# Kernel optimization log

Hardware: AMD Instinct MI355X
Metric: run time of the kernel (lower is better)

Reference implementation:

```python
import jax, jax.numpy as jnp
import numpy as np

CHUNK = 256
ROPE_BASE = 10000.0
EPS = 1e-6


def setup_inputs() -> dict:
    key = jax.random.key(0)
    ks = jax.random.split(key, 8)
    B, N, D, H, K = 4, 8192, 1024, 16, 4
    x = jax.random.normal(ks[0], (B, N, D), dtype=jnp.float32)
    norm_scale = jnp.ones((D,), dtype=jnp.float32)
    conv_w = jax.random.normal(ks[1], (D, 1, K), dtype=jnp.float32) * 0.2
    conv_b = jax.random.normal(ks[2], (D,), dtype=jnp.float32) * 0.02
    in_proj_w = jax.random.normal(ks[3], (D, 3 * D), dtype=jnp.float32) * 0.02
    dt_bias = jax.random.normal(ks[4], (D,), dtype=jnp.float32) * 0.5
    head_mix = jnp.eye(H, dtype=jnp.float32) + 0.02 * jax.random.normal(ks[5], (H, H), dtype=jnp.float32)
    out_proj_w = jax.random.normal(ks[6], (D, D), dtype=jnp.float32) * 0.02
    return {"x": x, "norm_scale": norm_scale, "conv_w": conv_w, "conv_b": conv_b,
            "in_proj_w": in_proj_w, "dt_bias": dt_bias, "head_mix": head_mix,
            "out_proj_w": out_proj_w}


def _rmsnorm(x, scale):
    xf = x.astype(jnp.float32)
    rms = jax.lax.rsqrt(jnp.mean(xf * xf, axis=-1, keepdims=True) + EPS)
    out = scale.astype(jnp.float32) * (xf * rms)
    return jnp.clip(out, -60000.0, 60000.0).astype(x.dtype)


def _rope(v, N, d_head, dtype):
    # v: (B, N, H, d_head); cos/sin: (N, d_head//2)
    half = d_head // 2
    inv_freq = 1.0 / (ROPE_BASE ** (jnp.arange(0, d_head, 2, dtype=jnp.float32) / d_head))
    freqs = jnp.arange(N, dtype=jnp.float32)[:, None] * inv_freq[None, :]
    cos = jnp.cos(freqs).astype(dtype)[None, :, None, :]
    sin = jnp.sin(freqs).astype(dtype)[None, :, None, :]
    v1, v2 = v[..., :half], v[..., half:]
    return jnp.concatenate([v1 * cos - v2 * sin, v1 * sin + v2 * cos], axis=-1)


def reference(x, norm_scale, conv_w, conv_b, in_proj_w, dt_bias, head_mix, out_proj_w):
    residual = x
    B, N, D = x.shape
    H = head_mix.shape[0]
    d_head = D // H
    xn = _rmsnorm(x, norm_scale)

    # depthwise causal conv: torch pads K-1 both sides then truncates to N -> left-pad only
    K = conv_w.shape[-1]
    xc = jax.lax.conv_general_dilated(
        xn.transpose(0, 2, 1), conv_w, window_strides=(1,), padding=[(K - 1, 0)],
        feature_group_count=D, dimension_numbers=("NCH", "OIH", "NCH"))
    xc = (xc + conv_b[None, :, None]).transpose(0, 2, 1)  # (B, N, D)
    xc = xc * jax.nn.sigmoid(xc)  # SiLU

    fused = xc @ in_proj_w  # (B, N, 3D)
    dt_raw, v, gate_raw = jnp.split(fused, 3, axis=-1)
    dt = jnp.clip(jax.nn.softplus(dt_raw.astype(jnp.float32) + dt_bias.astype(jnp.float32)),
                  0.001, 2.0).astype(dt_raw.dtype)
    gate = jax.nn.sigmoid(gate_raw)
    log_alpha = -dt.astype(jnp.float32)

    v_rot = _rope(v.reshape(B, N, H, d_head), N, d_head, x.dtype).reshape(B, N, D)
    v_in = (v_rot * dt).astype(jnp.float32)

    # pad to multiple of CHUNK (static)
    pad = (-N) % CHUNK
    if pad:
        v_in = jnp.pad(v_in, ((0, 0), (0, pad), (0, 0)))
        log_alpha = jnp.pad(log_alpha, ((0, 0), (0, pad), (0, 0)))
    Np = N + pad
    nc = Np // CHUNK
    v_ch = v_in.reshape(B, nc, CHUNK, D)
    la_ch = log_alpha.reshape(B, nc, CHUNK, D)

    # intra-chunk stabilized cumulative scan
    L = jnp.clip(jnp.cumsum(la_ch, axis=2), -20.0, 0.0)
    L_max = jnp.max(L, axis=2, keepdims=True)
    L_st = L - L_max
    cum_scaled = jnp.cumsum(jnp.exp(-L_st) * v_ch, axis=2)
    chunk_out = jnp.exp(L_st) * cum_scaled  # (B, nc, CHUNK, D)

    if nc > 1:
        # inter-chunk carry, fully parallel
        bdecay = L[:, :, -1, :]            # (B, nc, D)
        bout = chunk_out[:, :, -1, :]      # (B, nc, D)
        cum_decay = jnp.clip(jnp.cumsum(bdecay, axis=1), -80.0, 0.0)
        stab = jnp.max(cum_decay, axis=1, keepdims=True)
        ncd = jnp.clip(cum_decay - stab, -20.0, 0.0)
        seeds = bout * jnp.exp(-ncd)
        shifted = jnp.pad(seeds[:, :-1], ((0, 0), (1, 0), (0, 0)))
        carries = jnp.cumsum(shifted, axis=1) * jnp.exp(ncd)  # (B, nc, D)
        final = chunk_out + carries[:, :, None, :] * jnp.exp(L)
    else:
        final = chunk_out
    final = final.astype(x.dtype).reshape(B, Np, D)[:, :N, :]

    v_mix = jnp.einsum("bnhd,hm->bnmd", final.reshape(B, N, H, d_head), head_mix)
    final = v_mix.reshape(B, N, D)
    out = (final * gate) @ out_proj_w
    return residual + out
```

## Files before the change

### kernel.cpp

```cpp
#include <hip/hip_runtime.h>

#define TOK 32768
#define DMODEL 1024
#define NSEQ 8192
#define NCHK 32
#define CHUNKC 256
#define KDIM 1024
#define NKT (KDIM / 32)
#define LOG2E 1.44269504f

typedef __attribute__((ext_vector_type(8))) short bf16x8;
typedef __attribute__((ext_vector_type(4))) float f32x4;

__device__ __forceinline__ unsigned short f2bf(float f) {
  unsigned u = __float_as_uint(f);
  u += 0x7fffu + ((u >> 16) & 1u);
  return (unsigned short)(u >> 16);
}
__device__ __forceinline__ float bf2f(unsigned short h) {
  return __uint_as_float(((unsigned)h) << 16);
}
__device__ __forceinline__ float sigm(float x) {
  return __builtin_amdgcn_rcpf(1.f + exp2f(-LOG2E * x));
}

typedef __attribute__((address_space(3))) unsigned int lds_u32_t;
typedef const __attribute__((address_space(1))) unsigned int glb_u32_t;

__device__ __forceinline__ void gl_lds16(const void* g, void* l) {
  __builtin_amdgcn_global_load_lds((glb_u32_t*)g, (lds_u32_t*)l, 16, 0, 0);
}

__global__ __launch_bounds__(256) void transpose_bf16_k(const float* __restrict__ in,
                                                        unsigned short* __restrict__ out,
                                                        int R, int C) {
  __shared__ float tile[32][33];
  const int c0 = blockIdx.x * 32, r0 = blockIdx.y * 32;
  const int tx = threadIdx.x, ty = threadIdx.y;
#pragma unroll
  for (int i = 0; i < 32; i += 8)
    tile[ty + i][tx] = in[(long)(r0 + ty + i) * C + c0 + tx];
  __syncthreads();
#pragma unroll
  for (int i = 0; i < 32; i += 8)
    out[(long)(c0 + ty + i) * R + r0 + tx] = f2bf(tile[tx][ty + i]);
}

__global__ __launch_bounds__(256) void ropetab_k(float2* __restrict__ tab) {
  const int i = blockIdx.x * 256 + threadIdx.x;
  const int f = i & 31, n = i >> 5;
  const float invf = exp2f(-(float)f * (13.287712379549449f / 32.0f));
  const float ang = (float)n * invf;
  tab[i] = make_float2(cosf(ang), sinf(ang));
}

__global__ __launch_bounds__(256) void rmsconv_k(const float* __restrict__ x,
                                                 const float* __restrict__ scale,
                                                 const float* __restrict__ w,
                                                 const float* __restrict__ cb,
                                                 unsigned short* __restrict__ xc) {
  __shared__ float xs[11][1024];
  __shared__ float red[4];
  const int t = threadIdx.x;
  const long row0 = (long)blockIdx.x * 8;
  const bool seqstart = ((row0 & (NSEQ - 1)) == 0);
  const float4 sc = ((const float4*)scale)[t];
  for (int i = 0; i < 11; ++i) {
    if (i < 3 && seqstart) {
      ((float4*)xs[i])[t] = make_float4(0.f, 0.f, 0.f, 0.f);
      continue;
    }
    const long r = row0 - 3 + i;
    const float4 v = ((const float4*)(x + r * DMODEL))[t];
    float ss = v.x * v.x + v.y * v.y + v.z * v.z + v.w * v.w;
#pragma unroll
    for (int off = 32; off > 0; off >>= 1) ss += __shfl_down(ss, off);
    if ((t & 63) == 0) red[t >> 6] = ss;
    __syncthreads();
    const float tot = red[0] + red[1] + red[2] + red[3];
    const float rr = rsqrtf(tot * (1.0f / DMODEL) + 1e-6f);
    float4 o;
    o.x = fminf(fmaxf(v.x * rr * sc.x, -60000.f), 60000.f);
    o.y = fminf(fmaxf(v.y * rr * sc.y, -60000.f), 60000.f);
    o.z = fminf(fmaxf(v.z * rr * sc.z, -60000.f), 60000.f);
    o.w = fminf(fmaxf(v.w * rr * sc.w, -60000.f), 60000.f);
    ((float4*)xs[i])[t] = o;
    __syncthreads();
  }
  __syncthreads();
  const int d0 = t * 4;
  float wl[4][4];
#pragma unroll
  for (int j = 0; j < 4; ++j) {
    const float4 t4 = *(const float4*)(w + (d0 + j) * 4);
    wl[j][0] = t4.x; wl[j][1] = t4.y; wl[j][2] = t4.z; wl[j][3] = t4.w;
  }
  const float4 cb4 = ((const float4*)cb)[t];
#pragma unroll
  for (int orow = 0; orow < 8; ++orow) {
    float o[4] = {0.f, 0.f, 0.f, 0.f};
#pragma unroll
    for (int k = 0; k < 4; ++k) {
      const float4 xv = ((const float4*)xs[orow + k])[t];
      o[0] += xv.x * wl[0][k]; o[1] += xv.y * wl[1][k];
      o[2] += xv.z * wl[2][k]; o[3] += xv.w * wl[3][k];
    }
    ushort4 st;
    { const float a = o[0] + cb4.x; st.x = f2bf(a * sigm(a)); }
    { const float a = o[1] + cb4.y; st.y = f2bf(a * sigm(a)); }
    { const float a = o[2] + cb4.z; st.z = f2bf(a * sigm(a)); }
    { const float a = o[3] + cb4.w; st.w = f2bf(a * sigm(a)); }
    *(ushort4*)(xc + (row0 + orow) * DMODEL + d0) = st;
  }
}

template <int EPI, int NBN, int SBN>
__global__ __launch_bounds__(256) void gemm_bt(const unsigned short* __restrict__ A,
                                               const unsigned short* __restrict__ BT,
                                               unsigned short* __restrict__ ob,
                                               float* __restrict__ of,
                                               const float* __restrict__ resid) {
  __shared__ unsigned short As[3][128 * 32];
  __shared__ unsigned short Bs[3][256 * 32];
  const int tid = threadIdx.x;
  const int l = tid & 63;
  const int w = tid >> 6;
  constexpr int NC = (EPI == 0) ? 3072 : 1024;

  constexpr int BPS = 4 * SBN;
  constexpr int NBNS = NBN / SBN;
  const int lin = blockIdx.y * NBN + blockIdx.x;
  const int xcd = lin & 7;
  const int g = lin >> 3;
  const int s = g / BPS;
  const int r = g - s * BPS;
  const int bmo = r / SBN;
  const int bno = r - bmo * SBN;
  const int bmS = s / NBNS;
  const int bnS = s - bmS * NBNS;
  const int bm = xcd * 32 + bmS * 4 + bmo;
  const int bn = bnS * SBN + bno;

  f32x4 acc[8][4];
#pragma unroll
  for (int m = 0; m < 8; ++m)
#pragma unroll
    for (int n = 0; n < 4; ++n) acc[m][n] = {0.f, 0.f, 0.f, 0.f};

  const int srcc = (((l & 3) ^ ((l >> 3) & 3)) * 8);
  const unsigned short* aG0 = A + ((long)(bm * 128 + w * 32 + (l >> 2))) * KDIM + srcc;
  const unsigned short* bG0 = BT + ((long)(bn * 256 + w * 64 + (l >> 2))) * KDIM + srcc;
  const int aLo = (w * 32) * 32;
  const int bLo = (w * 64) * 32;

#define STAGE(buf, k0)                                           \
  {                                                              \
    gl_lds16(aG0 + (k0),             &As[buf][aLo]);             \
    gl_lds16(aG0 + (k0) + 16 * KDIM, &As[buf][aLo + 512]);       \
    gl_lds16(bG0 + (k0),             &Bs[buf][bLo]);             \
    gl_lds16(bG0 + (k0) + 16 * KDIM, &Bs[buf][bLo + 512]);       \
    gl_lds16(bG0 + (k0) + 32 * KDIM, &Bs[buf][bLo + 1024]);      \
    gl_lds16(bG0 + (k0) + 48 * KDIM, &Bs[buf][bLo + 1536]);      \
  }

  const int eoff = (((l >> 4) ^ ((l >> 1) & 3)) * 8);
  const int arow0 = (l & 15) * 32 + eoff;
  const int brow0 = (w * 64 + (l & 15)) * 32 + eoff;

  auto compute = [&](int cur) {
    const unsigned short* Ab = &As[cur][0];
    const unsigned short* Bb = &Bs[cur][0];
    bf16x8 af[8], bfr[4];
#pragma unroll
    for (int m = 0; m < 8; ++m) af[m] = *(const bf16x8*)&Ab[arow0 + m * 512];
#pragma unroll
    for (int n = 0; n < 4; ++n) bfr[n] = *(const bf16x8*)&Bb[brow0 + n * 512];
    __builtin_amdgcn_s_setprio(1);
#pragma unroll
    for (int m = 0; m < 8; ++m)
#pragma unroll
      for (int n = 0; n < 4; ++n)
        acc[m][n] = __builtin_amdgcn_mfma_f32_16x16x32_bf16(af[m], bfr[n], acc[m][n], 0, 0, 0);
    __builtin_amdgcn_s_setprio(0);
  };

  STAGE(0, 0);
  STAGE(1, 32);
  asm volatile("s_waitcnt vmcnt(6)" ::: "memory");
  int cur = 0, nxt = 2;
  for (int t = 0; t < NKT - 2; ++t) {
    __builtin_amdgcn_s_barrier();
    __builtin_amdgcn_sched_barrier(0);
    STAGE(nxt, (t + 2) * 32);
    compute(cur);
    asm volatile("s_waitcnt vmcnt(6)" ::: "memory");
    cur = (cur == 2) ? 0 : cur + 1;
    nxt = (nxt == 2) ? 0 : nxt + 1;
  }
  __builtin_amdgcn_s_barrier();
  __builtin_amdgcn_sched_barrier(0);
  compute(cur);
  asm volatile("s_waitcnt vmcnt(0)" ::: "memory");
  cur = (cur == 2) ? 0 : cur + 1;
  __builtin_amdgcn_s_barrier();
  __builtin_amdgcn_sched_barrier(0);
  compute(cur);
#undef STAGE

  const int rbase = bm * 128;
  const int cbase = bn * 256 + w * 64;
  const int lr4 = (l >> 4) * 4;
  const int lc16 = l & 15;

  if constexpr (EPI == 0) {
#pragma unroll
    for (int m = 0; m < 8; ++m)
#pragma unroll
      for (int n = 0; n < 4; ++n) {
        const int col = cbase + n * 16 + lc16;
#pragma unroll
        for (int j2 = 0; j2 < 4; ++j2) {
          const int row = rbase + m * 16 + lr4 + j2;
          ob[(long)row * NC + col] = f2bf(acc[m][n][j2]);
        }
      }
  } else {
#pragma unroll
    for (int m = 0; m < 8; ++m)
#pragma unroll
      for (int n = 0; n < 4; ++n) {
        const int col = cbase + n * 16 + lc16;
#pragma unroll
        for (int j2 = 0; j2 < 4; ++j2) {
          const int row = rbase + m * 16 + lr4 + j2;
          const long o = (long)row * NC + col;
          of[o] = resid[o] + acc[m][n][j2];
        }
      }
  }
}

__global__ __launch_bounds__(256) void scan1_k(const unsigned short* __restrict__ fu,
                                               const float* __restrict__ dt_bias,
                                               const float2* __restrict__ tab,
                                               float* __restrict__ Llast,
                                               float* __restrict__ bout) {
  const int idx = blockIdx.x * 256 + threadIdx.x;
  const int d = idx & 1023;
  const int ch = (idx >> 10) & 31;
  const int b = idx >> 15;
  const long base = ((long)b * NSEQ + ch * CHUNKC) * 3072 + d;
  const float bias = dt_bias[d];
  const int f = d & 31;
  const bool hi = (d & 32) != 0;
  const int po = hi ? -32 : 32;
  float run = 0.f, s = 0.f, L = 0.f;
#pragma unroll 4
  for (int c = 0; c < CHUNKC; ++c) {
    const long o = base + (long)c * 3072;
    const float a = bf2f(fu[o]) + bias;
    const float e2 = exp2f(-LOG2E * fabsf(a));
    const float sp = fmaxf(a, 0.f) + 0.69314718f * log2f(1.f + e2);
    const float dtv = fminf(fmaxf(sp, 0.001f), 2.0f);
    const float own = bf2f(fu[o + 1024]);
    const float oth = bf2f(fu[o + 1024 + po]);
    const float2 cs = tab[(ch * CHUNKC + c) * 32 + f];
    const float vr = own * cs.x + (hi ? oth * cs.y : -oth * cs.y);
    run -= dtv;
    L = fminf(fmaxf(run, -20.f), 0.f);
    s += exp2f(-LOG2E * L) * (vr * dtv);
  }
  Llast[idx] = L;
  bout[idx] = exp2f(LOG2E * L) * s;
}

__global__ __launch_bounds__(256) void scan2_k(const float* __restrict__ Llast,
                                               const float* __restrict__ bout,
                                               float* __restrict__ carry) {
  const int idx = blockIdx.x * 256 + threadIdx.x;
  const int d = idx & 1023;
  const int b = idx >> 10;
  const long base = (long)b * (NCHK * DMODEL) + d;
  float cd[NCHK];
  float run = 0.f, stab = -1e30f;
#pragma unroll
  for (int ch = 0; ch < NCHK; ++ch) {
    run += Llast[base + ch * DMODEL];
    cd[ch] = fminf(fmaxf(run, -80.f), 0.f);
    stab = fmaxf(stab, cd[ch]);
  }
  float acc = 0.f;
#pragma unroll
  for (int ch = 0; ch < NCHK; ++ch) {
    const float ncd = fminf(fmaxf(cd[ch] - stab, -20.f), 0.f);
    carry[base + ch * DMODEL] = acc * exp2f(LOG2E * ncd);
    acc += bout[base + ch * DMODEL] * exp2f(-LOG2E * ncd);
  }
}

__global__ __launch_bounds__(256) void scan3_k(unsigned short* fu,
                                               const float* __restrict__ dt_bias,
                                               const float2* __restrict__ tab,
                                               const float* __restrict__ carry) {
  const int idx = blockIdx.x * 256 + threadIdx.x;
  const int d = idx & 1023;
  const int ch = (idx >> 10) & 31;
  const int b = idx >> 15;
  const long base = ((long)b * NSEQ + ch * CHUNKC) * 3072 + d;
  const float bias = dt_bias[d];
  const int f = d & 31;
  const bool hi = (d & 32) != 0;
  const int po = hi ? -32 : 32;
  const float ce = carry[idx];
  float run = 0.f, s = 0.f;
#pragma unroll 4
  for (int c = 0; c < CHUNKC; ++c) {
    const long o = base + (long)c * 3072;
    const float a = bf2f(fu[o]) + bias;
    const float e2 = exp2f(-LOG2E * fabsf(a));
    const float sp = fmaxf(a, 0.f) + 0.69314718f * log2f(1.f + e2);
    const float dtv = fminf(fmaxf(sp, 0.001f), 2.0f);
    const float own = bf2f(fu[o + 1024]);
    const float oth = bf2f(fu[o + 1024 + po]);
    const float2 cs = tab[(ch * CHUNKC + c) * 32 + f];
    const float vr = own * cs.x + (hi ? oth * cs.y : -oth * cs.y);
    run -= dtv;
    const float L = fminf(fmaxf(run, -20.f), 0.f);
    s += exp2f(-LOG2E * L) * (vr * dtv);
    fu[o + 1024] = f2bf(exp2f(LOG2E * L) * (s + ce));
  }
}

__global__ __launch_bounds__(256) void headmix_k(const unsigned short* __restrict__ fu,
                                                 const float* __restrict__ hm,
                                                 unsigned short* __restrict__ A2) {
  __shared__ float mixs[256];
  const int t = threadIdx.x;
  mixs[t] = hm[t];
  __syncthreads();
  const long row = (long)blockIdx.x * 4 + (t >> 6);
  const int dd = t & 63;
  const unsigned short* fv0 = fu + row * 3072 + 1024 + dd;
  const unsigned short* gv0 = fu + row * 3072 + 2048 + dd;
  float fv[16];
#pragma unroll
  for (int h = 0; h < 16; ++h) fv[h] = bf2f(fv0[h * 64]);
#pragma unroll
  for (int m = 0; m < 16; ++m) {
    float o = 0.f;
#pragma unroll
    for (int h = 0; h < 16; ++h) o += fv[h] * mixs[h * 16 + m];
    A2[row * DMODEL + m * 64 + dd] = f2bf(o * sigm(bf2f(gv0[m * 64])));
  }
}

extern "C" void kernel_launch(void* const* d_in, const int* in_sizes, int n_in,
                              void* d_out, int out_size, void* d_ws, size_t ws_size,
                              hipStream_t stream) {
  const float* x        = (const float*)d_in[0];
  const float* nscale   = (const float*)d_in[1];
  const float* conv_w   = (const float*)d_in[2];
  const float* conv_b   = (const float*)d_in[3];
  const float* in_proj  = (const float*)d_in[4];
  const float* dt_bias  = (const float*)d_in[5];
  const float* head_mix = (const float*)d_in[6];
  const float* out_proj = (const float*)d_in[7];
  float* out = (float*)d_out;

  char* p = (char*)d_ws;
  unsigned short* W1T = (unsigned short*)p; p += (size_t)3072 * 1024 * 2;
  unsigned short* W2T = (unsigned short*)p; p += (size_t)1024 * 1024 * 2;
  float2* tab  = (float2*)p; p += (size_t)NSEQ * 32 * sizeof(float2);
  float* Llast = (float*)p;  p += (size_t)131072 * 4;
  float* bout  = (float*)p;  p += (size_t)131072 * 4;
  float* carry = (float*)p;  p += (size_t)131072 * 4;
  unsigned short* fusedb = (unsigned short*)p; p += (size_t)TOK * 3072 * 2;
  unsigned short* xc     = (unsigned short*)p; p += (size_t)TOK * DMODEL * 2;

  transpose_bf16_k<<<dim3(96, 32), dim3(32, 8), 0, stream>>>(in_proj, W1T, 1024, 3072);
  transpose_bf16_k<<<dim3(32, 32), dim3(32, 8), 0, stream>>>(out_proj, W2T, 1024, 1024);
  ropetab_k<<<1024, 256, 0, stream>>>(tab);
  rmsconv_k<<<TOK / 8, 256, 0, stream>>>(x, nscale, conv_w, conv_b, xc);

  gemm_bt<0, 12, 6><<<dim3(12, 256), 256, 0, stream>>>(xc, W1T, fusedb, nullptr, nullptr);
  scan1_k<<<512, 256, 0, stream>>>(fusedb, dt_bias, tab, Llast, bout);
  scan2_k<<<16, 256, 0, stream>>>(Llast, bout, carry);
  scan3_k<<<512, 256, 0, stream>>>(fusedb, dt_bias, tab, carry);
  headmix_k<<<TOK / 4, 256, 0, stream>>>(fusedb, head_mix, xc );
  gemm_bt<1, 4, 4><<<dim3(4, 256), 256, 0, stream>>>(xc, W2T, nullptr, out, x);
}
```

Baseline: 626.8 us.

## Enlarge GEMM tiles to 256x256 with 8 waves, fuse prep kernels, register-resident rmsconv

The GEMM moves from 128x256 tiles with 4 waves to 256x256 tiles with 8 waves arranged 2x4, with per-wave staging adjusted. This halves the grid and increases operand reuse per LDS load. The weight transposes and the rope table are merged into one prep launch. rmsconv now keeps its 11 input rows in registers and does a single barrier instead of staging through 44KB of LDS. The risks are higher register pressure and fewer blocks per CU for the GEMM.

```diff
diff --git a/kernel.cpp b/kernel.cpp
--- a/kernel.cpp
+++ b/kernel.cpp
@@ -6,7 +6,6 @@
 #define NCHK 32
 #define CHUNKC 256
 #define KDIM 1024
-#define NKT (KDIM / 32)
 #define LOG2E 1.44269504f
 
 typedef __attribute__((ext_vector_type(8))) short bf16x8;
@@ -31,27 +30,36 @@
   __builtin_amdgcn_global_load_lds((glb_u32_t*)g, (lds_u32_t*)l, 16, 0, 0);
 }
 
-__global__ __launch_bounds__(256) void transpose_bf16_k(const float* __restrict__ in,
-                                                        unsigned short* __restrict__ out,
-                                                        int R, int C) {
+__global__ __launch_bounds__(256) void prep_k(const float* __restrict__ w1,
+                                              const float* __restrict__ w2,
+                                              unsigned short* __restrict__ w1t,
+                                              unsigned short* __restrict__ w2t,
+                                              float2* __restrict__ tab) {
   __shared__ float tile[32][33];
-  const int c0 = blockIdx.x * 32, r0 = blockIdx.y * 32;
-  const int tx = threadIdx.x, ty = threadIdx.y;
-#pragma unroll
-  for (int i = 0; i < 32; i += 8)
-    tile[ty + i][tx] = in[(long)(r0 + ty + i) * C + c0 + tx];
-  __syncthreads();
-#pragma unroll
-  for (int i = 0; i < 32; i += 8)
-    out[(long)(c0 + ty + i) * R + r0 + tx] = f2bf(tile[tx][ty + i]);
-}
-
-__global__ __launch_bounds__(256) void ropetab_k(float2* __restrict__ tab) {
-  const int i = blockIdx.x * 256 + threadIdx.x;
-  const int f = i & 31, n = i >> 5;
-  const float invf = exp2f(-(float)f * (13.287712379549449f / 32.0f));
-  const float ang = (float)n * invf;
-  tab[i] = make_float2(cosf(ang), sinf(ang));
+  const int bid = blockIdx.x;
+  const int t = threadIdx.x;
+  if (bid < 4096) {
+    const float* in;
+    unsigned short* out;
+    int c0, r0;
+    if (bid < 3072) { in = w1; out = w1t; c0 = (bid % 96) * 32; r0 = (bid / 96) * 32; }
+    else            { in = w2; out = w2t; c0 = ((bid - 3072) & 31) * 32; r0 = ((bid - 3072) >> 5) * 32; }
+    const int C = (bid < 3072) ? 3072 : 1024;
+    const int tx = t & 31, ty = t >> 5;
+#pragma unroll
+    for (int i = 0; i < 32; i += 8)
+      tile[ty + i][tx] = in[(long)(r0 + ty + i) * C + c0 + tx];
+    __syncthreads();
+#pragma unroll
+    for (int i = 0; i < 32; i += 8)
+      out[(long)(c0 + ty + i) * 1024 + r0 + tx] = f2bf(tile[tx][ty + i]);
+  } else {
+    const int i = (bid - 4096) * 256 + t;
+    const int f = i & 31, n = i >> 5;
+    const float invf = exp2f(-(float)f * (13.287712379549449f / 32.0f));
+    const float ang = (float)n * invf;
+    tab[i] = make_float2(cosf(ang), sinf(ang));
+  }
 }
 
 __global__ __launch_bounds__(256) void rmsconv_k(const float* __restrict__ x,
@@ -59,35 +67,34 @@
                                                  const float* __restrict__ w,
                                                  const float* __restrict__ cb,
                                                  unsigned short* __restrict__ xc) {
-  __shared__ float xs[11][1024];
-  __shared__ float red[4];
+  __shared__ float red[11][4];
   const int t = threadIdx.x;
   const long row0 = (long)blockIdx.x * 8;
   const bool seqstart = ((row0 & (NSEQ - 1)) == 0);
   const float4 sc = ((const float4*)scale)[t];
+  float4 vr[11];
+#pragma unroll
   for (int i = 0; i < 11; ++i) {
     if (i < 3 && seqstart) {
-      ((float4*)xs[i])[t] = make_float4(0.f, 0.f, 0.f, 0.f);
-      continue;
+      vr[i] = make_float4(0.f, 0.f, 0.f, 0.f);
+    } else {
+      vr[i] = ((const float4*)(x + (row0 - 3 + i) * DMODEL))[t];
     }
-    const long r = row0 - 3 + i;
-    const float4 v = ((const float4*)(x + r * DMODEL))[t];
-    float ss = v.x * v.x + v.y * v.y + v.z * v.z + v.w * v.w;
+    float ss = vr[i].x * vr[i].x + vr[i].y * vr[i].y + vr[i].z * vr[i].z + vr[i].w * vr[i].w;
 #pragma unroll
     for (int off = 32; off > 0; off >>= 1) ss += __shfl_down(ss, off);
-    if ((t & 63) == 0) red[t >> 6] = ss;
-    __syncthreads();
-    const float tot = red[0] + red[1] + red[2] + red[3];
+    if ((t & 63) == 0) red[i][t >> 6] = ss;
+  }
+  __syncthreads();
+#pragma unroll
+  for (int i = 0; i < 11; ++i) {
+    const float tot = red[i][0] + red[i][1] + red[i][2] + red[i][3];
     const float rr = rsqrtf(tot * (1.0f / DMODEL) + 1e-6f);
-    float4 o;
-    o.x = fminf(fmaxf(v.x * rr * sc.x, -60000.f), 60000.f);
-    o.y = fminf(fmaxf(v.y * rr * sc.y, -60000.f), 60000.f);
-    o.z = fminf(fmaxf(v.z * rr * sc.z, -60000.f), 60000.f);
-    o.w = fminf(fmaxf(v.w * rr * sc.w, -60000.f), 60000.f);
-    ((float4*)xs[i])[t] = o;
-    __syncthreads();
-  }
-  __syncthreads();
+    vr[i].x = fminf(fmaxf(vr[i].x * rr * sc.x, -60000.f), 60000.f);
+    vr[i].y = fminf(fmaxf(vr[i].y * rr * sc.y, -60000.f), 60000.f);
+    vr[i].z = fminf(fmaxf(vr[i].z * rr * sc.z, -60000.f), 60000.f);
+    vr[i].w = fminf(fmaxf(vr[i].w * rr * sc.w, -60000.f), 60000.f);
+  }
   const int d0 = t * 4;
   float wl[4][4];
 #pragma unroll
@@ -101,7 +108,7 @@
     float o[4] = {0.f, 0.f, 0.f, 0.f};
 #pragma unroll
     for (int k = 0; k < 4; ++k) {
-      const float4 xv = ((const float4*)xs[orow + k])[t];
+      const float4 xv = vr[orow + k];
       o[0] += xv.x * wl[0][k]; o[1] += xv.y * wl[1][k];
       o[2] += xv.z * wl[2][k]; o[3] += xv.w * wl[3][k];
     }
@@ -115,17 +122,19 @@
 }
 
 template <int EPI, int NBN, int SBN>
-__global__ __launch_bounds__(256) void gemm_bt(const unsigned short* __restrict__ A,
+__global__ __launch_bounds__(512) void gemm_bt(const unsigned short* __restrict__ A,
                                                const unsigned short* __restrict__ BT,
                                                unsigned short* __restrict__ ob,
                                                float* __restrict__ of,
                                                const float* __restrict__ resid) {
-  __shared__ unsigned short As[3][128 * 32];
-  __shared__ unsigned short Bs[3][256 * 32];
+  __shared__ unsigned short As[3][8192];
+  __shared__ unsigned short Bs[3][8192];
   const int tid = threadIdx.x;
   const int l = tid & 63;
   const int w = tid >> 6;
+  const int wr = w >> 2, wc = w & 3;
   constexpr int NC = (EPI == 0) ? 3072 : 1024;
+  constexpr int NKT = KDIM / 32;
 
   constexpr int BPS = 4 * SBN;
   constexpr int NBNS = NBN / SBN;
@@ -138,7 +147,7 @@
   const int bno = r - bmo * SBN;
   const int bmS = s / NBNS;
   const int bnS = s - bmS * NBNS;
-  const int bm = xcd * 32 + bmS * 4 + bmo;
+  const int bm = xcd * 16 + bmS * 4 + bmo;
   const int bn = bnS * SBN + bno;
 
   f32x4 acc[8][4];
@@ -148,33 +157,28 @@
     for (int n = 0; n < 4; ++n) acc[m][n] = {0.f, 0.f, 0.f, 0.f};
 
   const int srcc = (((l & 3) ^ ((l >> 3) & 3)) * 8);
-  const unsigned short* aG0 = A + ((long)(bm * 128 + w * 32 + (l >> 2))) * KDIM + srcc;
-  const unsigned short* bG0 = BT + ((long)(bn * 256 + w * 64 + (l >> 2))) * KDIM + srcc;
-  const int aLo = (w * 32) * 32;
-  const int bLo = (w * 64) * 32;
-
-#define STAGE(buf, k0)                                           \
-  {                                                              \
-    gl_lds16(aG0 + (k0),             &As[buf][aLo]);             \
-    gl_lds16(aG0 + (k0) + 16 * KDIM, &As[buf][aLo + 512]);       \
-    gl_lds16(bG0 + (k0),             &Bs[buf][bLo]);             \
-    gl_lds16(bG0 + (k0) + 16 * KDIM, &Bs[buf][bLo + 512]);       \
-    gl_lds16(bG0 + (k0) + 32 * KDIM, &Bs[buf][bLo + 1024]);      \
-    gl_lds16(bG0 + (k0) + 48 * KDIM, &Bs[buf][bLo + 1536]);      \
-  }
+  const unsigned short* aG0 = A + ((long)(bm * 256 + w * 32 + (l >> 2))) * KDIM + srcc;
+  const unsigned short* bG0 = BT + ((long)(bn * 256 + w * 32 + (l >> 2))) * KDIM + srcc;
+  const int wL0 = w * 1024;
+
+#define STAGE(buf, k0)                                          \
+  { gl_lds16(aG0 + (k0),            &As[buf][wL0]);             \
+    gl_lds16(aG0 + (k0) + 16*KDIM,  &As[buf][wL0 + 512]);       \
+    gl_lds16(bG0 + (k0),            &Bs[buf][wL0]);             \
+    gl_lds16(bG0 + (k0) + 16*KDIM,  &Bs[buf][wL0 + 512]); }
 
   const int eoff = (((l >> 4) ^ ((l >> 1) & 3)) * 8);
-  const int arow0 = (l & 15) * 32 + eoff;
-  const int brow0 = (w * 64 + (l & 15)) * 32 + eoff;
+  const int aRowOff = (wr * 128 + (l & 15)) * 32 + eoff;
+  const int bRowOff = (wc * 64 + (l & 15)) * 32 + eoff;
 
   auto compute = [&](int cur) {
     const unsigned short* Ab = &As[cur][0];
     const unsigned short* Bb = &Bs[cur][0];
     bf16x8 af[8], bfr[4];
 #pragma unroll
-    for (int m = 0; m < 8; ++m) af[m] = *(const bf16x8*)&Ab[arow0 + m * 512];
-#pragma unroll
-    for (int n = 0; n < 4; ++n) bfr[n] = *(const bf16x8*)&Bb[brow0 + n * 512];
+    for (int m = 0; m < 8; ++m) af[m] = *(const bf16x8*)&Ab[aRowOff + m * 512];
+#pragma unroll
+    for (int n = 0; n < 4; ++n) bfr[n] = *(const bf16x8*)&Bb[bRowOff + n * 512];
     __builtin_amdgcn_s_setprio(1);
 #pragma unroll
     for (int m = 0; m < 8; ++m)
@@ -186,14 +190,14 @@
 
   STAGE(0, 0);
   STAGE(1, 32);
-  asm volatile("s_waitcnt vmcnt(6)" ::: "memory");
+  asm volatile("s_waitcnt vmcnt(4)" ::: "memory");
   int cur = 0, nxt = 2;
   for (int t = 0; t < NKT - 2; ++t) {
     __builtin_amdgcn_s_barrier();
     __builtin_amdgcn_sched_barrier(0);
     STAGE(nxt, (t + 2) * 32);
     compute(cur);
-    asm volatile("s_waitcnt vmcnt(6)" ::: "memory");
+    asm volatile("s_waitcnt vmcnt(4)" ::: "memory");
     cur = (cur == 2) ? 0 : cur + 1;
     nxt = (nxt == 2) ? 0 : nxt + 1;
   }
@@ -207,8 +211,8 @@
   compute(cur);
 #undef STAGE
 
-  const int rbase = bm * 128;
-  const int cbase = bn * 256 + w * 64;
+  const int rbase = bm * 256 + wr * 128;
+  const int cbase = bn * 256 + wc * 64;
   const int lr4 = (l >> 4) * 4;
   const int lc16 = l & 15;
 
@@ -377,15 +381,13 @@
   unsigned short* fusedb = (unsigned short*)p; p += (size_t)TOK * 3072 * 2;
   unsigned short* xc     = (unsigned short*)p; p += (size_t)TOK * DMODEL * 2;
 
-  transpose_bf16_k<<<dim3(96, 32), dim3(32, 8), 0, stream>>>(in_proj, W1T, 1024, 3072);
-  transpose_bf16_k<<<dim3(32, 32), dim3(32, 8), 0, stream>>>(out_proj, W2T, 1024, 1024);
-  ropetab_k<<<1024, 256, 0, stream>>>(tab);
+  prep_k<<<5120, 256, 0, stream>>>(in_proj, out_proj, W1T, W2T, tab);
   rmsconv_k<<<TOK / 8, 256, 0, stream>>>(x, nscale, conv_w, conv_b, xc);
 
-  gemm_bt<0, 12, 6><<<dim3(12, 256), 256, 0, stream>>>(xc, W1T, fusedb, nullptr, nullptr);
+  gemm_bt<0, 12, 6><<<dim3(12, 128), 512, 0, stream>>>(xc, W1T, fusedb, nullptr, nullptr);
   scan1_k<<<512, 256, 0, stream>>>(fusedb, dt_bias, tab, Llast, bout);
   scan2_k<<<16, 256, 0, stream>>>(Llast, bout, carry);
   scan3_k<<<512, 256, 0, stream>>>(fusedb, dt_bias, tab, carry);
   headmix_k<<<TOK / 4, 256, 0, stream>>>(fusedb, head_mix, xc );
-  gemm_bt<1, 4, 4><<<dim3(4, 256), 256, 0, stream>>>(xc, W2T, nullptr, out, x);
-}
+  gemm_bt<1, 4, 4><<<dim3(4, 128), 512, 0, stream>>>(xc, W2T, nullptr, out, x);
+}
```

Measured after the change: 654.4 us. 4.4% more time.
